# Kernel tuning notes

Hardware: AMD Instinct MI355X
Metric: run time of the kernel (lower is better)

Reference implementation:

```python
import jax, jax.numpy as jnp
import numpy as np

DIM = 1024
DEPTH = 4
HEADS = 16
DIM_HEAD = 64
INNER = HEADS * DIM_HEAD  # 1024
FF_INNER = 4 * DIM
EPS = 1e-5


def _layer_norm(x, g, b):
    mu = jnp.mean(x, axis=-1, keepdims=True)
    var = jnp.mean(jnp.square(x - mu), axis=-1, keepdims=True)
    return (x - mu) * jax.lax.rsqrt(var + EPS) * g + b


def setup_inputs() -> dict:
    key = jax.random.key(0)
    ks = jax.random.split(key, 8)
    s = 0.02
    return {
        "x": jax.random.normal(ks[0], (2, 2048, DIM), dtype=jnp.float32),
        "mask": jnp.ones((2, 2048), dtype=bool),
        "ln1_g": jnp.ones((DEPTH, DIM), jnp.float32),
        "ln1_b": jnp.zeros((DEPTH, DIM), jnp.float32),
        "wqkv": jax.random.normal(ks[1], (DEPTH, DIM, 3 * INNER), jnp.float32) * s,
        "wo": jax.random.normal(ks[2], (DEPTH, INNER, DIM), jnp.float32) * s,
        "ln2_g": jnp.ones((DEPTH, DIM), jnp.float32),
        "ln2_b": jnp.zeros((DEPTH, DIM), jnp.float32),
        "w1": jax.random.normal(ks[3], (DEPTH, DIM, FF_INNER), jnp.float32) * s,
        "b1": jnp.zeros((DEPTH, FF_INNER), jnp.float32),
        "w2": jax.random.normal(ks[4], (DEPTH, FF_INNER, DIM), jnp.float32) * s,
        "b2": jnpp if False else jnp.zeros((DEPTH, DIM), jnp.float32),
    }


def _attention(x, mask, wqkv, wo):
    b, n, _ = x.shape
    qkv = x @ wqkv  # [b, n, 3*inner]
    q, k, v = jnp.split(qkv, 3, axis=-1)
    def heads(t):
        return t.reshape(b, n, HEADS, DIM_HEAD).transpose(0, 2, 1, 3)  # b h n d
    q, k, v = heads(q), heads(k), heads(v)
    scale = DIM_HEAD ** -0.5
    dots = jnp.einsum('bhid,bhjd->bhij', q, k) * scale
    neg = -jnp.finfo(dots.dtype).max
    dots = jnp.where(mask[:, None, None, :], dots, neg)
    attn = jax.nn.softmax(dots, axis=-1)
    out = jnp.einsum('bhij,bhjd->bhid', attn, v)
    out = out.transpose(0, 2, 1, 3).reshape(b, n, INNER)
    return out @ wo


def reference(x, mask, ln1_g, ln1_b, wqkv, wo, ln2_g, ln2_b, w1, b1, w2, b2):
    for l in range(DEPTH):
        x = _attention(_layer_norm(x, ln1_g[l], ln1_b[l]), mask, wqkv[l], wo[l]) + x
        h = _layer_norm(x, ln2_g[l], ln2_b[l])
        h = jax.nn.gelu(h @ w1[l] + b1[l], approximate=False) @ w2[l] + b2[l]
        x = h + x
    return x
```

## Files before the change

kernel.cpp:

```cpp
#include <hip/hip_runtime.h>

using u16 = unsigned short;
typedef __attribute__((ext_vector_type(8))) short short8;
typedef __attribute__((ext_vector_type(4))) short short4v;
typedef __attribute__((ext_vector_type(4))) float floatx4;

#define SEQ   2048
#define NROWS 4096
#define NDIM  1024
#define QKV_N 3072
#define FF_N  4096

__device__ __forceinline__ u16 f2bf(float f) {
  unsigned u = __builtin_bit_cast(unsigned, f);
  u += 0x7FFFu + ((u >> 16) & 1u);
  return (u16)(u >> 16);
}
__device__ __forceinline__ u16 f2bt(float f) {
  return (u16)(__builtin_bit_cast(unsigned, f) >> 16);
}
__device__ __forceinline__ float bf2f(u16 h) {
  unsigned u = ((unsigned)h) << 16;
  return __builtin_bit_cast(float, u);
}

__device__ __forceinline__ void gl_lds16(const void* g, void* l) {
  __builtin_amdgcn_global_load_lds(
      (const __attribute__((address_space(1))) unsigned int*)(uintptr_t)g,
      (__attribute__((address_space(3))) unsigned int*)(uintptr_t)l, 16, 0, 0);
}

__launch_bounds__(256)
__global__ void kconv4(const float* __restrict__ in_qkv,
                       const float* __restrict__ in_wo,
                       const float* __restrict__ in_w1,
                       const float* __restrict__ in_w2,
                       u16* __restrict__ o_qkv, u16* __restrict__ o_wo,
                       u16* __restrict__ o_w1, u16* __restrict__ o_w2) {
  int bid = blockIdx.x;
  const float* in;
  u16* out;
  int K, N, tx, ty;
  if (bid < 768) {
    in = in_qkv; out = o_qkv; K = 1024; N = 3072; tx = bid % 48; ty = bid / 48;
  } else if (bid < 1024) {
    int r = bid - 768;
    in = in_wo; out = o_wo; K = 1024; N = 1024; tx = r % 16; ty = r / 16;
  } else if (bid < 2048) {
    int r = bid - 1024;
    in = in_w1; out = o_w1; K = 1024; N = 4096; tx = r % 64; ty = r / 64;
  } else {
    int r = bid - 2048;
    in = in_w2; out = o_w2; K = 4096; N = 1024; tx = r % 16; ty = r / 16;
  }
  __shared__ float tile[64][65];
  int k0 = ty * 64, n0 = tx * 64;
  int t = threadIdx.x;
  int lrow = t >> 4;
  int lc4 = (t & 15) * 4;
#pragma unroll
  for (int r = 0; r < 4; r++) {
    int k = lrow + r * 16;
    float4 v = *(const float4*)&in[(size_t)(k0 + k) * N + n0 + lc4];
    tile[k][lc4 + 0] = v.x;
    tile[k][lc4 + 1] = v.y;
    tile[k][lc4 + 2] = v.z;
    tile[k][lc4 + 3] = v.w;
  }
  __syncthreads();
  int n = t >> 2;
  int kc = (t & 3) * 16;
  short8 o0, o1;
#pragma unroll
  for (int j = 0; j < 8; j++) o0[j] = (short)f2bf(tile[kc + j][n]);
#pragma unroll
  for (int j = 0; j < 8; j++) o1[j] = (short)f2bf(tile[kc + 8 + j][n]);
  *(short8*)&out[(size_t)(n0 + n) * K + k0 + kc] = o0;
  *(short8*)&out[(size_t)(n0 + n) * K + k0 + kc + 8] = o1;
}

__launch_bounds__(256)
__global__ void kln(const float* __restrict__ x, const float* __restrict__ g,
                    const float* __restrict__ b, u16* __restrict__ out) {
  int t = threadIdx.x, l = t & 63, w = t >> 6;
  int row = blockIdx.x * 4 + w;
  const float* xr = x + (size_t)row * NDIM;
  float4 v[4];
  float s = 0.f, ss = 0.f;
#pragma unroll
  for (int j = 0; j < 4; j++) {
    v[j] = *(const float4*)&xr[(l + 64 * j) * 4];
    s += v[j].x + v[j].y + v[j].z + v[j].w;
    ss += v[j].x * v[j].x + v[j].y * v[j].y + v[j].z * v[j].z + v[j].w * v[j].w;
  }
#pragma unroll
  for (int m = 1; m < 64; m <<= 1) {
    s += __shfl_xor(s, m);
    ss += __shfl_xor(ss, m);
  }
  float mu = s * (1.0f / NDIM);
  float rs = rsqrtf(ss * (1.0f / NDIM) - mu * mu + 1e-5f);
#pragma unroll
  for (int j = 0; j < 4; j++) {
    float4 gv = *(const float4*)&g[(l + 64 * j) * 4];
    float4 bv = *(const float4*)&b[(l + 64 * j) * 4];
    short4v ov;
    ov[0] = (short)f2bf((v[j].x - mu) * rs * gv.x + bv.x);
    ov[1] = (short)f2bf((v[j].y - mu) * rs * gv.y + bv.y);
    ov[2] = (short)f2bf((v[j].z - mu) * rs * gv.z + bv.z);
    ov[3] = (short)f2bf((v[j].w - mu) * rs * gv.w + bv.w);
    *(short4v*)&out[(size_t)row * NDIM + (l + 64 * j) * 4] = ov;
  }
}

template <int EPI>
__launch_bounds__(512, 2)
__global__ void kgemm256(const u16* __restrict__ A, const u16* __restrict__ Bt,
                         int K, int N, const float* __restrict__ bias,
                         void* __restrict__ out, void* __restrict__ out2,
                         void* __restrict__ out3) {
  __shared__ __align__(16) char ldsA[2][32768];
  __shared__ __align__(16) char ldsB[2][32768];
  int nx = gridDim.x;
  int id = blockIdx.y * nx + blockIdx.x;
  int cpx = (nx * gridDim.y) >> 3;
  int sw = (id & 7) * cpx + (id >> 3);
  int m0 = (sw % nx) * 256;
  int n0 = (sw / nx) * 256;
  int t = threadIdx.x;
  int l = t & 63, w = t >> 6;
  int wmrow = (w >> 2) * 128;
  int wnrow = (w & 3) * 64;
  int lr = l & 15;
  int lg = l >> 4;
  int NT2 = K >> 6;

  int srcsw = ((l & 7) ^ (l >> 3)) * 8;
  auto stageA = [&](int tile, int u) {
    char* dst = ldsA[tile & 1] + u * 1024;
    gl_lds16(&A[(size_t)(m0 + u * 8 + (l >> 3)) * K + (tile << 6) + srcsw], dst);
  };
  auto stageB = [&](int tile, int u) {
    char* dst = ldsB[tile & 1] + u * 1024;
    gl_lds16(&Bt[(size_t)(n0 + u * 8 + (l >> 3)) * K + (tile << 6) + srcsw], dst);
  };
  auto slot = [&](int tile, int s) {
    if (tile >= NT2) return;
    int e0 = 2 * w, e1 = 2 * w + 1;
    if (s == 0) {
      stageA(tile, e0 < 8 ? e0 : e0 + 8);
      stageA(tile, e1 < 8 ? e1 : e1 + 8);
    } else if (s == 1) {
      stageB(tile, (e0 >> 2) * 8 + (e0 & 3));
      stageB(tile, (e1 >> 2) * 8 + (e1 & 3));
    } else if (s == 2) {
      stageB(tile, (e0 >> 2) * 8 + 4 + (e0 & 3));
      stageB(tile, (e1 >> 2) * 8 + 4 + (e1 & 3));
    } else {
      stageA(tile, e0 < 8 ? e0 + 8 : e0 + 16);
      stageA(tile, e1 < 8 ? e1 + 8 : e1 + 16);
    }
  };

  floatx4 acc[8][4];
#pragma unroll
  for (int m = 0; m < 8; m++)
#pragma unroll
    for (int n = 0; n < 4; n++) acc[m][n] = (floatx4){0.f, 0.f, 0.f, 0.f};

  short8 af[4][2], bf0[2][2], bf1[2][2];
  auto loadAg = [&](int buf, int mg) {
#pragma unroll
    for (int mf = 0; mf < 4; mf++)
#pragma unroll
      for (int kh = 0; kh < 2; kh++) {
        int row = wmrow + (mg * 4 + mf) * 16 + lr;
        int ch = (kh * 4 + lg) ^ (row & 7);
        af[mf][kh] = *(const short8*)(ldsA[buf] + row * 128 + ch * 16);
      }
  };
  auto loadBg = [&](int buf, short8 (&bb)[2][2], int ng) {
#pragma unroll
    for (int nf = 0; nf < 2; nf++)
#pragma unroll
      for (int kh = 0; kh < 2; kh++) {
        int row = wnrow + (ng * 2 + nf) * 16 + lr;
        int ch = (kh * 4 + lg) ^ (row & 7);
        bb[nf][kh] = *(const short8*)(ldsB[buf] + row * 128 + ch * 16);
      }
  };
  auto doQ = [&](int mg, short8 (&bb)[2][2], int ng) {
    __builtin_amdgcn_s_setprio(1);
#pragma unroll
    for (int mf = 0; mf < 4; mf++)
#pragma unroll
      for (int nf = 0; nf < 2; nf++)
#pragma unroll
        for (int kh = 0; kh < 2; kh++)
          acc[mg * 4 + mf][ng * 2 + nf] =
              __builtin_amdgcn_mfma_f32_16x16x32_bf16(
                  af[mf][kh], bb[nf][kh], acc[mg * 4 + mf][ng * 2 + nf], 0, 0, 0);
    __builtin_amdgcn_s_setprio(0);
  };
#define FENCE asm volatile("" ::: "memory")
#define BAR __builtin_amdgcn_s_barrier()

#pragma unroll
  for (int s = 0; s < 4; s++) slot(0, s);
#pragma unroll
  for (int s = 0; s < 4; s++) slot(1, s);
  asm volatile("s_waitcnt vmcnt(0)" ::: "memory");
  BAR;

  int NI = NT2 >> 1;
  for (int i = 0; i < NI; i++) {
    int t0 = 2 * i, t1 = 2 * i + 1;
    loadAg(0, 0); loadBg(0, bf0, 0); FENCE;
    if (i > 0) slot(t1, 3);
    BAR; doQ(0, bf0, 0); BAR;
    loadBg(0, bf1, 1); FENCE;
    slot(t0 + 2, 0);
    BAR; doQ(0, bf1, 1); BAR;
    loadAg(0, 1); FENCE;
    slot(t0 + 2, 1);
    BAR; doQ(1, bf0, 0); BAR;
    slot(t0 + 2, 2);
    if (t0 + 2 < NT2) asm volatile("s_waitcnt vmcnt(6)" ::: "memory");
    else              asm volatile("s_waitcnt vmcnt(0)" ::: "memory");
    BAR; doQ(1, bf1, 1); BAR;
    loadAg(1, 0); loadBg(1, bf0, 0); FENCE;
    slot(t0 + 2, 3);
    BAR; doQ(0, bf0, 0); BAR;
    loadBg(1, bf1, 1); FENCE;
    slot(t1 + 2, 0);
    BAR; doQ(0, bf1, 1); BAR;
    loadAg(1, 1); FENCE;
    slot(t1 + 2, 1);
    BAR; doQ(1, bf0, 0); BAR;
    slot(t1 + 2, 2);
    if (t1 + 2 < NT2) asm volatile("s_waitcnt vmcnt(6)" ::: "memory");
    BAR; doQ(1, bf1, 1); BAR;
  }
#undef FENCE
#undef BAR

  int lq = lg * 4;
#pragma unroll
  for (int m = 0; m < 8; m++)
#pragma unroll
    for (int n = 0; n < 4; n++) {
      int row0 = m0 + wmrow + m * 16 + lq;
      int col = n0 + wnrow + n * 16 + lr;
      if (EPI == 4) {
        int bb = row0 >> 11, s = row0 & 2047;
        if (col < 2048) {
          int h = (col & 1023) >> 6, d = col & 63;
          u16* dst = (col < 1024) ? (u16*)out : (u16*)out2;
          size_t base = ((size_t)(bb * 16 + h) * SEQ + s) * 64 + d;
#pragma unroll
          for (int i2 = 0; i2 < 4; i2++)
            dst[base + (size_t)i2 * 64] = f2bf(acc[m][n][i2]);
        } else {
          int h = (col - 2048) >> 6, d = col & 63;
          short4v pv;
#pragma unroll
          for (int i2 = 0; i2 < 4; i2++) pv[i2] = (short)f2bf(acc[m][n][i2]);
          *(short4v*)&((u16*)out3)[((size_t)(bb * 16 + h) * 64 + d) * SEQ + s] = pv;
        }
      } else {
#pragma unroll
        for (int i2 = 0; i2 < 4; i2++) {
          float v = acc[m][n][i2] + bias[col];
          v = 0.5f * v * (1.0f + erff(v * 0.70710678118f));
          ((u16*)out)[(size_t)(row0 + i2) * N + col] = f2bf(v);
        }
      }
    }
}

#define BM 128
#define BN 128
#define BK 32

template <int EPI>
__launch_bounds__(256, 3)
__global__ void kgemm(const u16* __restrict__ A, const u16* __restrict__ Bt,
                      int K, int N, const float* __restrict__ bias,
                      const float* __restrict__ res, void* __restrict__ out) {
  __shared__ __align__(16) u16 As[3][BM * BK];
  __shared__ __align__(16) u16 Bs[3][BN * BK];
  int nx = gridDim.x;
  int id = blockIdx.y * nx + blockIdx.x;
  int cpx = (nx * gridDim.y) >> 3;
  int sw = (id & 7) * cpx + (id >> 3);
  int m0 = (sw % nx) * BM;
  int n0 = (sw / nx) * BN;
  int t = threadIdx.x;
  int l = t & 63, w = t >> 6;
  int wm = (w >> 1) * 64, wn = (w & 1) * 64;
  int lr = l & 15;

  int c16 = (l >> 4) * 16;
  int offA[4], offB[4];
#pragma unroll
  for (int m = 0; m < 4; m++) {
    int lin = (wm + m * 16 + lr) * 64 + c16;
    offA[m] = lin ^ (((lin >> 7) & 7) << 4);
  }
#pragma unroll
  for (int n = 0; n < 4; n++) {
    int lin = (wn + n * 16 + lr) * 64 + c16;
    offB[n] = lin ^ (((lin >> 7) & 7) << 4);
  }

  auto stage = [&](int tt, int bf) {
    int kk = tt << 5;
#pragma unroll
    for (int p = 0; p < 2; p++) {
      int u0 = p * 256 + w * 64;
      int u = u0 + l;
      int lin = (u * 16) ^ (((u >> 3) & 7) << 4);
      int row = lin >> 6;
      int col = (lin & 63) >> 1;
      gl_lds16(&A[(size_t)(m0 + row) * K + kk + col], (char*)As[bf] + u0 * 16);
      gl_lds16(&Bt[(size_t)(n0 + row) * K + kk + col], (char*)Bs[bf] + u0 * 16);
    }
  };

  floatx4 acc[4][4];
#pragma unroll
  for (int m = 0; m < 4; m++)
#pragma unroll
    for (int n = 0; n < 4; n++) acc[m][n] = (floatx4){0.f, 0.f, 0.f, 0.f};

  int NT = K >> 5;
  stage(0, 0);
  stage(1, 1);
  int ra = 0, rb = 1, rc = 2;

  for (int tt = 0; tt < NT; ++tt) {
    if (tt + 2 < NT) {
      stage(tt + 2, rc);
      asm volatile("s_waitcnt vmcnt(8)" ::: "memory");
    } else if (tt + 1 < NT) {
      asm volatile("s_waitcnt vmcnt(4)" ::: "memory");
    } else {
      asm volatile("s_waitcnt vmcnt(0)" ::: "memory");
    }
    __builtin_amdgcn_s_barrier();
    const char* Ab = (const char*)As[ra];
    const char* Bb = (const char*)Bs[ra];
    short8 af[4], bfr[4];
#pragma unroll
    for (int m = 0; m < 4; m++) af[m] = *(const short8*)(Ab + offA[m]);
#pragma unroll
    for (int n = 0; n < 4; n++) bfr[n] = *(const short8*)(Bb + offB[n]);
    __builtin_amdgcn_s_setprio(1);
#pragma unroll
    for (int m = 0; m < 4; m++)
#pragma unroll
      for (int n = 0; n < 4; n++)
        acc[m][n] = __builtin_amdgcn_mfma_f32_16x16x32_bf16(af[m], bfr[n],
                                                            acc[m][n], 0, 0, 0);
    __builtin_amdgcn_s_setprio(0);
    __builtin_amdgcn_s_barrier();
    int tmp = ra; ra = rb; rb = rc; rc = tmp;
  }

  int lq = (l >> 4) * 4;
#pragma unroll
  for (int m = 0; m < 4; m++)
#pragma unroll
    for (int n = 0; n < 4; n++)
#pragma unroll
      for (int i = 0; i < 4; i++) {
        int row = m0 + wm + m * 16 + lq + i;
        int col = n0 + wn + n * 16 + lr;
        float v = acc[m][n][i];
        if (EPI == 2) {
          v += res[(size_t)row * N + col];
          ((float*)out)[(size_t)row * N + col] = v;
        } else {
          v += bias[col] + res[(size_t)row * N + col];
          ((float*)out)[(size_t)row * N + col] = v;
        }
      }
}

#define KSTR 72
__launch_bounds__(256, 4)
__global__ void kflash(const u16* __restrict__ Qb, const u16* __restrict__ Kb,
                       const u16* __restrict__ Vb, u16* __restrict__ ao) {
  __shared__ __align__(16) u16 Ks[64 * 64];
  __shared__ __align__(16) u16 Vt[64 * 64];
  __shared__ __align__(16) u16 Ps[4][16 * KSTR];
  int t = threadIdx.x, l = t & 63, w = t >> 6;
  int bid = blockIdx.x;
  int xcd = bid & 7, sslot = bid >> 3;
  int bh = xcd + 8 * (sslot >> 5);
  int qc = sslot & 31;
  int b = bh >> 4, h = bh & 15;
  int q0 = qc * 64 + w * 16;
  int lr = l & 15, g = l >> 4, lk = g * 8;
  const u16* qbase = Qb + (size_t)(b * 16 + h) * SEQ * 64;
  const u16* kbase = Kb + (size_t)(b * 16 + h) * SEQ * 64;
  const u16* vbase = Vb + (size_t)(b * 16 + h) * 64 * SEQ;

  const float QSC = 0.125f * 1.44269504f;
  short8 qf[2];
#pragma unroll
  for (int k2 = 0; k2 < 2; k2++) {
    short8 v = *(const short8*)(qbase + (size_t)(q0 + lr) * 64 + k2 * 32 + lk);
#pragma unroll
    for (int j = 0; j < 8; j++) v[j] = (short)f2bf(bf2f((u16)v[j]) * QSC);
    qf[k2] = v;
  }

  short8 onesb;
#pragma unroll
  for (int j = 0; j < 8; j++) onesb[j] = (lr == 0) ? (short)0x3F80 : (short)0;

  floatx4 o[4], ol;
  float mrow[4];
  ol = (floatx4){0.f, 0.f, 0.f, 0.f};
#pragma unroll
  for (int n = 0; n < 4; n++) o[n] = (floatx4){0.f, 0.f, 0.f, 0.f};
#pragma unroll
  for (int i = 0; i < 4; i++) mrow[i] = -1e30f;

  for (int kv = 0; kv < SEQ; kv += 64) {
    __syncthreads();
#pragma unroll
    for (int p = 0; p < 2; p++) {
      int u0 = p * 256 + w * 64;
      int r = (u0 + l) >> 3;
      int cs = ((l & 7) ^ (r & 7)) * 8;
      gl_lds16(kbase + (size_t)(kv + r) * 64 + cs, &Ks[(size_t)u0 * 8]);
      gl_lds16(vbase + (size_t)r * SEQ + kv + cs, &Vt[(size_t)u0 * 8]);
    }
    __syncthreads();

    floatx4 s[4];
#pragma unroll
    for (int n = 0; n < 4; n++) s[n] = (floatx4){0.f, 0.f, 0.f, 0.f};
    __builtin_amdgcn_s_setprio(1);
#pragma unroll
    for (int n = 0; n < 4; n++)
#pragma unroll
      for (int k2 = 0; k2 < 2; k2++) {
        int row = n * 16 + lr;
        int byte = (row * 128 + (k2 * 32 + lk) * 2) ^ ((row & 7) << 4);
        short8 kb = *(const short8*)((const char*)Ks + byte);
        s[n] = __builtin_amdgcn_mfma_f32_16x16x32_bf16(qf[k2], kb, s[n], 0, 0, 0);
      }
    __builtin_amdgcn_s_setprio(0);

    float pmax[4];
    bool need = false;
#pragma unroll
    for (int i = 0; i < 4; i++) {
      float mx = fmaxf(fmaxf(s[0][i], s[1][i]), fmaxf(s[2][i], s[3][i]));
      pmax[i] = mx;
      need |= (mx > mrow[i] + 11.0f);
    }
    if (__any(need)) {
#pragma unroll
      for (int i = 0; i < 4; i++) {
        float mx = pmax[i];
#pragma unroll
        for (int d = 1; d < 16; d <<= 1) mx = fmaxf(mx, __shfl_xor(mx, d));
        float nm = fmaxf(mrow[i], mx);
        float corr = __builtin_amdgcn_exp2f(mrow[i] - nm);
        mrow[i] = nm;
#pragma unroll
        for (int n = 0; n < 4; n++) o[n][i] *= corr;
        ol[i] *= corr;
      }
    }
#pragma unroll
    for (int i = 0; i < 4; i++) {
      int prow = (g * 4 + i) * KSTR;
#pragma unroll
      for (int n = 0; n < 4; n++)
        Ps[w][prow + n * 16 + lr] = f2bt(__builtin_amdgcn_exp2f(s[n][i] - mrow[i]));
    }

    short8 pa[2];
#pragma unroll
    for (int k2 = 0; k2 < 2; k2++)
      pa[k2] = *(const short8*)&Ps[w][lr * KSTR + k2 * 32 + lk];
    __builtin_amdgcn_s_setprio(1);
#pragma unroll
    for (int n = 0; n < 4; n++)
#pragma unroll
      for (int k2 = 0; k2 < 2; k2++) {
        int d = n * 16 + lr;
        int byte = (d * 128 + (k2 * 32 + lk) * 2) ^ ((d & 7) << 4);
        short8 vb = *(const short8*)((const char*)Vt + byte);
        o[n] = __builtin_amdgcn_mfma_f32_16x16x32_bf16(pa[k2], vb, o[n], 0, 0, 0);
      }
#pragma unroll
    for (int k2 = 0; k2 < 2; k2++)
      ol = __builtin_amdgcn_mfma_f32_16x16x32_bf16(pa[k2], onesb, ol, 0, 0, 0);
    __builtin_amdgcn_s_setprio(0);
  }

#pragma unroll
  for (int i = 0; i < 4; i++) {
    float lsum = __shfl(ol[i], l & 48);
    float inv = 1.0f / lsum;
    int grow = b * SEQ + q0 + g * 4 + i;
#pragma unroll
    for (int n = 0; n < 4; n++)
      ao[(size_t)grow * NDIM + h * 64 + n * 16 + lr] = f2bt(o[n][i] * inv);
  }
}

extern "C" void kernel_launch(void* const* d_in, const int* in_sizes, int n_in,
                              void* d_out, int out_size, void* d_ws,
                              size_t ws_size, hipStream_t stream) {
  const float* x = (const float*)d_in[0];
  const float* ln1_g = (const float*)d_in[2];
  const float* ln1_b = (const float*)d_in[3];
  const float* wqkv = (const float*)d_in[4];
  const float* wo = (const float*)d_in[5];
  const float* ln2_g = (const float*)d_in[6];
  const float* ln2_b = (const float*)d_in[7];
  const float* w1 = (const float*)d_in[8];
  const float* b1 = (const float*)d_in[9];
  const float* w2 = (const float*)d_in[10];
  const float* b2 = (const float*)d_in[11];
  float* xout = (float*)d_out;

  char* ws = (char*)d_ws;
  size_t off = 0;
  auto alloc = [&](size_t bytes) {
    void* p = ws + off;
    off += (bytes + 255) & ~(size_t)255;
    return p;
  };
  u16* wqkv_t = (u16*)alloc((size_t)QKV_N * NDIM * 2);
  u16* wo_t = (u16*)alloc((size_t)NDIM * NDIM * 2);
  u16* w1_t = (u16*)alloc((size_t)FF_N * NDIM * 2);
  u16* w2_t = (u16*)alloc((size_t)NDIM * FF_N * 2);
  u16* actA = (u16*)alloc((size_t)NROWS * NDIM * 2);
  u16* actB = (u16*)alloc((size_t)NROWS * NDIM * 2);
  u16* big = (u16*)alloc((size_t)NROWS * FF_N * 2);
  u16* Qb = (u16*)alloc((size_t)NROWS * NDIM * 2);
  u16* Kbuf = (u16*)alloc((size_t)NROWS * NDIM * 2);
  u16* Vbuf = (u16*)alloc((size_t)NROWS * NDIM * 2);

  for (int lyr = 0; lyr < 4; lyr++) {
    const float* xin = (lyr == 0) ? x : xout;

    kconv4<<<dim3(3072), 256, 0, stream>>>(
        wqkv + (size_t)lyr * NDIM * QKV_N, wo + (size_t)lyr * NDIM * NDIM,
        w1 + (size_t)lyr * NDIM * FF_N, w2 + (size_t)lyr * FF_N * NDIM,
        wqkv_t, wo_t, w1_t, w2_t);

    kln<<<NROWS / 4, 256, 0, stream>>>(xin, ln1_g + lyr * NDIM,
                                       ln1_b + lyr * NDIM, actA);
    kgemm256<4><<<dim3(NROWS / 256, QKV_N / 256), 512, 0, stream>>>(
        actA, wqkv_t, NDIM, QKV_N, nullptr, Qb, Kbuf, Vbuf);
    kflash<<<dim3(1024), 256, 0, stream>>>(Qb, Kbuf, Vbuf, actB);
    kgemm<2><<<dim3(NROWS / BM, NDIM / BN), 256, 0, stream>>>(
        actB, wo_t, NDIM, NDIM, nullptr, xin, xout);
    kln<<<NROWS / 4, 256, 0, stream>>>(xout, ln2_g + lyr * NDIM,
                                       ln2_b + lyr * NDIM, actA);
    kgemm256<1><<<dim3(NROWS / 256, FF_N / 256), 512, 0, stream>>>(
        actA, w1_t, NDIM, FF_N, b1 + (size_t)lyr * FF_N, big, nullptr, nullptr);
    kgemm<3><<<dim3(NROWS / BM, NDIM / BN), 256, 0, stream>>>(
        big, w2_t, FF_N, NDIM, b2 + (size_t)lyr * NDIM, xout, xout);
  }
}
```

Before: 942.2 us.

## Transpose QK^T MFMA so each lane owns one query row in attention softmax

Swaps the MFMA operands so S is computed transposed and each lane holds scores for a single query row. The per-row max then reduces within registers plus two cross-lane shuffles instead of four 16-lane butterfly reductions. The running max becomes a scalar, and P is written to LDS as packed 8-byte stores instead of scattered 2-byte stores. The rescale path now needs shuffles to hand the correction factors back to the output-accumulator layout.

```diff
diff --git a/kernel.cpp b/kernel.cpp
--- a/kernel.cpp
+++ b/kernel.cpp
@@ -421,12 +421,10 @@
   for (int j = 0; j < 8; j++) onesb[j] = (lr == 0) ? (short)0x3F80 : (short)0;
 
   floatx4 o[4], ol;
-  float mrow[4];
+  float mrow = -1e30f;
   ol = (floatx4){0.f, 0.f, 0.f, 0.f};
 #pragma unroll
   for (int n = 0; n < 4; n++) o[n] = (floatx4){0.f, 0.f, 0.f, 0.f};
-#pragma unroll
-  for (int i = 0; i < 4; i++) mrow[i] = -1e30f;
 
   for (int kv = 0; kv < SEQ; kv += 64) {
     __syncthreads();
@@ -451,38 +449,42 @@
         int row = n * 16 + lr;
         int byte = (row * 128 + (k2 * 32 + lk) * 2) ^ ((row & 7) << 4);
         short8 kb = *(const short8*)((const char*)Ks + byte);
-        s[n] = __builtin_amdgcn_mfma_f32_16x16x32_bf16(qf[k2], kb, s[n], 0, 0, 0);
+        s[n] = __builtin_amdgcn_mfma_f32_16x16x32_bf16(kb, qf[k2], s[n], 0, 0, 0);
       }
     __builtin_amdgcn_s_setprio(0);
 
-    float pmax[4];
-    bool need = false;
-#pragma unroll
-    for (int i = 0; i < 4; i++) {
-      float mx = fmaxf(fmaxf(s[0][i], s[1][i]), fmaxf(s[2][i], s[3][i]));
-      pmax[i] = mx;
-      need |= (mx > mrow[i] + 11.0f);
-    }
-    if (__any(need)) {
-#pragma unroll
-      for (int i = 0; i < 4; i++) {
-        float mx = pmax[i];
-#pragma unroll
-        for (int d = 1; d < 16; d <<= 1) mx = fmaxf(mx, __shfl_xor(mx, d));
-        float nm = fmaxf(mrow[i], mx);
-        float corr = __builtin_amdgcn_exp2f(mrow[i] - nm);
-        mrow[i] = nm;
-#pragma unroll
-        for (int n = 0; n < 4; n++) o[n][i] *= corr;
-        ol[i] *= corr;
-      }
-    }
-#pragma unroll
-    for (int i = 0; i < 4; i++) {
-      int prow = (g * 4 + i) * KSTR;
+    float mx = s[0][0];
+#pragma unroll
+    for (int n = 0; n < 4; n++)
+#pragma unroll
+      for (int i = 0; i < 4; i++) mx = fmaxf(mx, s[n][i]);
+    mx = fmaxf(mx, __shfl_xor(mx, 16));
+    mx = fmaxf(mx, __shfl_xor(mx, 32));
+    if (__any(mx > mrow + 11.0f)) {
+      float nm = fmaxf(mrow, mx);
+      float corr = __builtin_amdgcn_exp2f(mrow - nm);
+      mrow = nm;
+      float c4[4];
+#pragma unroll
+      for (int i = 0; i < 4; i++) c4[i] = __shfl(corr, g * 4 + i);
 #pragma unroll
       for (int n = 0; n < 4; n++)
-        Ps[w][prow + n * 16 + lr] = f2bt(__builtin_amdgcn_exp2f(s[n][i] - mrow[i]));
+#pragma unroll
+        for (int i = 0; i < 4; i++) o[n][i] *= c4[i];
+#pragma unroll
+      for (int i = 0; i < 4; i++) ol[i] *= c4[i];
+    }
+
+#pragma unroll
+    for (int n = 0; n < 4; n++) {
+      float p0 = __builtin_amdgcn_exp2f(s[n][0] - mrow);
+      float p1 = __builtin_amdgcn_exp2f(s[n][1] - mrow);
+      float p2 = __builtin_amdgcn_exp2f(s[n][2] - mrow);
+      float p3 = __builtin_amdgcn_exp2f(s[n][3] - mrow);
+      uint2 pr;
+      pr.x = (unsigned)f2bt(p0) | ((unsigned)f2bt(p1) << 16);
+      pr.y = (unsigned)f2bt(p2) | ((unsigned)f2bt(p3) << 16);
+      *(uint2*)((char*)Ps[w] + (size_t)(lr * KSTR + n * 16 + g * 4) * 2) = pr;
     }
 
     short8 pa[2];
```

Result: no change. 939.3 us (-0.3%).
